# Optimization experiments

Hardware: AMD Instinct MI355X
Metric: run time of the kernel (lower is better)

The kernel has to match this reference:

```python
import jax, jax.numpy as jnp
import numpy as np

M, K, N = 131072, 1024, 512


def setup_inputs() -> dict:
    key = jax.random.key(0)
    k1, k2, k3, k4, k5 = jax.random.split(key, 5)
    scale = 0.02
    return {
        "x": jax.random.normal(k1, (M, K), dtype=jnp.float32),
        "w0": jax.random.uniform(k2, (K,), dtype=jnp.float32, minval=0.9, maxval=1.1),
        "w1": jax.random.normal(k3, (K, N), dtype=jnp.float32) * scale,
        "w2": jax.random.normal(k4, (K, N), dtype=jnp.float32) * scale,
        "w3": jax.random.normal(k5, (N, K), dtype=jnp.float32) * scale,
    }


def reference(x, w0, w1, w2, w3):
    # RMSNorm (no eps, matching the kernel): l = rsqrt(mean(x^2))
    l = jax.lax.rsqrt(jnp.sum(x * x, axis=-1) / K)          # [M]
    x1 = x * l[:, None] * w0[None, :]                        # [M, K]
    x2 = x1 @ w1                                             # gate   [M, N]
    y2 = x1 @ w2                                             # up     [M, N]
    x3 = jax.nn.silu(x2) * y2                                # SiLU-gate [M, N]
    out = x3 @ w3                                            # down   [M, K] (skip_connection=False)
    return out
```

## Files before the change

### kernel.cpp

```cpp
#include <hip/hip_runtime.h>
#include <cstdint>

typedef __attribute__((ext_vector_type(4))) float f32x4;
typedef __attribute__((ext_vector_type(8))) short bf16x8;
typedef __attribute__((ext_vector_type(4))) short bf16x4;

#define DEV static __device__ __forceinline__

DEV unsigned short f2bf(float f) {
    union { float f; unsigned int u; } v; v.f = f;
    unsigned int u = v.u;
    return (unsigned short)((u + 0x7FFFu + ((u >> 16) & 1u)) >> 16);
}

DEV void async_cp16(const void* g, void* l) {
    __builtin_amdgcn_global_load_lds(
        (const __attribute__((address_space(1))) unsigned int*)g,
        (__attribute__((address_space(3))) unsigned int*)l,
        16, 0, 0);
}

DEV void stage_half(const unsigned short* __restrict__ g, long kofs,
                    unsigned short* l, int tid, int gpitch) {
#pragma unroll
    for (int i = 0; i < 2; ++i) {
        int c = i * 512 + tid;
        int row = c >> 3;
        int ss = (c & 7) ^ (row & 7);
        async_cp16(g + (long)row * gpitch + kofs + ss * 8,
                   l + (i * 512 + (tid & 448)) * 8);
    }
}

template <int NT>
DEV void gemm256(const unsigned short* __restrict__ gA,
                 const unsigned short* __restrict__ gB,
                 const int gpitch, unsigned short* lds,
                 f32x4 (&acc)[8][4], const int tid) {
    const int lane = tid & 63;
    const int wv = tid >> 6;
    const int wr = wv >> 2;
    const int wcq = wv & 3;
    const int lhi = lane >> 4, llo = lane & 15;
    const int hb = wcq >> 1;
    const int br0 = (wcq & 1) * 64;

#define MFMA8(AF, BF, RI0, CJ0)                                               \
    _Pragma("unroll") for (int kq = 0; kq < 2; ++kq)                          \
    _Pragma("unroll") for (int i = 0; i < 4; ++i)                             \
    _Pragma("unroll") for (int j = 0; j < 2; ++j)                             \
        acc[RI0 + i][CJ0 + j] = __builtin_amdgcn_mfma_f32_16x16x32_bf16(      \
            AF[kq][i], BF[kq][j], acc[RI0 + i][CJ0 + j], 0, 0, 0);

#pragma unroll
    for (int h = 0; h < 2; ++h) {
        stage_half(gA + (long)h * 128 * gpitch, 0, lds + h * 8192, tid, gpitch);
        stage_half(gB + (long)h * 128 * gpitch, 0, lds + 32768 + h * 8192, tid, gpitch);
    }
    asm volatile("s_waitcnt vmcnt(0)" ::: "memory");
    __builtin_amdgcn_s_barrier();

    bf16x8 af[2][4], bf0[2][2], bf1[2][2];

    for (int kt = 0; kt < NT; ++kt) {
        const int cur = kt & 1, nxt = cur ^ 1;
        const unsigned short* lA = lds + (cur * 2 + wr) * 8192;
        const unsigned short* lB = lds + 32768 + (cur * 2 + hb) * 8192;
        const bool pf = (kt + 1 < NT);
        const long kofs = (long)(kt + 1) * 64;

#pragma unroll
        for (int kq = 0; kq < 2; ++kq) {
            const int q = kq * 4 + lhi;
#pragma unroll
            for (int i = 0; i < 4; ++i) {
                int r = i * 16 + llo;
                af[kq][i] = *(const bf16x8*)&lA[r * 64 + ((q ^ (r & 7)) << 3)];
            }
#pragma unroll
            for (int j = 0; j < 2; ++j) {
                int r = br0 + j * 16 + llo;
                bf0[kq][j] = *(const bf16x8*)&lB[r * 64 + ((q ^ (r & 7)) << 3)];
            }
        }
        if (pf) {
            stage_half(gA, kofs, lds + (nxt * 2 + 0) * 8192, tid, gpitch);
            stage_half(gA + (long)128 * gpitch, kofs, lds + (nxt * 2 + 1) * 8192, tid, gpitch);
        }
        __builtin_amdgcn_s_barrier();
        asm volatile("s_waitcnt lgkmcnt(0)");
        __builtin_amdgcn_sched_barrier(0);
        __builtin_amdgcn_s_setprio(1);
        MFMA8(af, bf0, 0, 0)
        __builtin_amdgcn_s_setprio(0);
        __builtin_amdgcn_s_barrier();

#pragma unroll
        for (int kq = 0; kq < 2; ++kq) {
            const int q = kq * 4 + lhi;
#pragma unroll
            for (int j = 0; j < 2; ++j) {
                int r = br0 + 32 + j * 16 + llo;
                bf1[kq][j] = *(const bf16x8*)&lB[r * 64 + ((q ^ (r & 7)) << 3)];
            }
        }
        if (pf) {
            stage_half(gB, kofs, lds + 32768 + (nxt * 2 + 0) * 8192, tid, gpitch);
            stage_half(gB + (long)128 * gpitch, kofs, lds + 32768 + (nxt * 2 + 1) * 8192, tid, gpitch);
        }
        __builtin_amdgcn_s_barrier();
        asm volatile("s_waitcnt lgkmcnt(0)");
        __builtin_amdgcn_sched_barrier(0);
        __builtin_amdgcn_s_setprio(1);
        MFMA8(af, bf1, 0, 2)
        __builtin_amdgcn_s_setprio(0);
        __builtin_amdgcn_s_barrier();

#pragma unroll
        for (int kq = 0; kq < 2; ++kq) {
            const int q = kq * 4 + lhi;
#pragma unroll
            for (int i = 0; i < 4; ++i) {
                int r = 64 + i * 16 + llo;
                af[kq][i] = *(const bf16x8*)&lA[r * 64 + ((q ^ (r & 7)) << 3)];
            }
        }
        __builtin_amdgcn_s_barrier();
        asm volatile("s_waitcnt lgkmcnt(0)");
        __builtin_amdgcn_sched_barrier(0);
        __builtin_amdgcn_s_setprio(1);
        MFMA8(af, bf0, 4, 0)
        __builtin_amdgcn_s_setprio(0);
        __builtin_amdgcn_s_barrier();

        __builtin_amdgcn_s_setprio(1);
        MFMA8(af, bf1, 4, 2)
        __builtin_amdgcn_s_setprio(0);
        if (pf) asm volatile("s_waitcnt vmcnt(0)" ::: "memory");
        __builtin_amdgcn_s_barrier();
        __builtin_amdgcn_sched_barrier(0);
    }
#undef MFMA8
}

__global__ void prep_w(const float* __restrict__ w0, const float* __restrict__ w1,
                       const float* __restrict__ w2, const float* __restrict__ w3,
                       unsigned short* __restrict__ w12t, unsigned short* __restrict__ w3t) {
    int t = blockIdx.x * 256 + threadIdx.x;
    if (t < 1048576) {
        int n = t >> 10, k = t & 1023;
        const float* src = (n & 1) ? w2 : w1;
        w12t[t] = f2bf(w0[k] * src[k * 512 + (n >> 1)]);
    } else {
        int idx = t - 1048576;
        int j = idx >> 9, n = idx & 511;
        w3t[idx] = f2bf(w3[n * 1024 + j]);
    }
}

__global__ __launch_bounds__(256)
void prep_x(const float* __restrict__ x, unsigned short* __restrict__ xb) {
    const int wv = threadIdx.x >> 6, lane = threadIdx.x & 63;
    const int stride = gridDim.x * 4;
    for (int row = blockIdx.x * 4 + wv; row < 131072; row += stride) {
        const float* xr = x + (long)row * 1024;
        f32x4 v[4];
        float s = 0.f;
#pragma unroll
        for (int c = 0; c < 4; ++c) {
            v[c] = *(const f32x4*)(xr + c * 256 + lane * 4);
            s += v[c].x * v[c].x + v[c].y * v[c].y + v[c].z * v[c].z + v[c].w * v[c].w;
        }
#pragma unroll
        for (int off = 32; off > 0; off >>= 1) s += __shfl_xor(s, off, 64);
        float l = rsqrtf(s * (1.0f / 1024.0f));
        unsigned short* xo = xb + (long)row * 1024;
#pragma unroll
        for (int c = 0; c < 4; ++c) {
            bf16x4 b;
            b.x = (short)f2bf(v[c].x * l);
            b.y = (short)f2bf(v[c].y * l);
            b.z = (short)f2bf(v[c].z * l);
            b.w = (short)f2bf(v[c].w * l);
            *(bf16x4*)(xo + c * 256 + lane * 4) = b;
        }
    }
}

__global__ __launch_bounds__(512, 2)
void gate_gemm(const unsigned short* __restrict__ xb,
               const unsigned short* __restrict__ w12t,
               unsigned short* __restrict__ x3) {
    __shared__ unsigned short lds[65536];
    const int tid = threadIdx.x;
    const int lane = tid & 63;
    const int wv = tid >> 6;
    const int wr = wv >> 2, wcq = wv & 3;
    const int lhi = lane >> 4, llo = lane & 15;

    int bid = blockIdx.x;
    int wgid = (bid & 7) * 256 + (bid >> 3);
    const int mt = wgid >> 2, nt = wgid & 3;

    f32x4 acc[8][4];
#pragma unroll
    for (int i = 0; i < 8; ++i)
#pragma unroll
        for (int j = 0; j < 4; ++j) acc[i][j] = (f32x4){0.f, 0.f, 0.f, 0.f};

    gemm256<16>(xb + (long)mt * 256 * 1024, w12t + (long)nt * 256 * 1024,
                1024, lds, acc, tid);

#pragma unroll
    for (int ri = 0; ri < 8; ++ri)
#pragma unroll
        for (int rr = 0; rr < 4; ++rr) {
            int R = wr * 128 + ri * 16 + lhi * 4 + rr;
#pragma unroll
            for (int cj = 0; cj < 4; ++cj) {
                float v = acc[ri][cj][rr];
                float p = __shfl_xor(v, 1, 64);
                float g = (lane & 1) ? p : v;
                float u = (lane & 1) ? v : p;
                float s = (g / (1.0f + __expf(-g))) * u;
                if (!(lane & 1))
                    lds[R * 136 + wcq * 32 + cj * 8 + (llo >> 1)] = f2bf(s);
            }
        }
    __syncthreads();
    unsigned short* xg = x3 + (long)(mt * 256) * 512 + nt * 128;
#pragma unroll
    for (int i = 0; i < 8; ++i) {
        int c = i * 512 + tid;
        int row = c >> 4, ch = c & 15;
        *(bf16x8*)(xg + (long)row * 512 + ch * 8) = *(const bf16x8*)&lds[row * 136 + ch * 8];
    }
}

__global__ __launch_bounds__(512, 2)
void down_gemm(const unsigned short* __restrict__ x3,
               const unsigned short* __restrict__ w3t,
               float* __restrict__ out) {
    __shared__ unsigned short lds[65536];
    const int tid = threadIdx.x;
    const int lane = tid & 63;
    const int wv = tid >> 6;
    const int wr = wv >> 2, wcq = wv & 3;
    const int lhi = lane >> 4, llo = lane & 15;

    int bid = blockIdx.x;
    int wgid = (bid & 7) * 256 + (bid >> 3);
    const int mt = wgid >> 2, nt = wgid & 3;

    f32x4 acc[8][4];
#pragma unroll
    for (int i = 0; i < 8; ++i)
#pragma unroll
        for (int j = 0; j < 4; ++j) acc[i][j] = (f32x4){0.f, 0.f, 0.f, 0.f};

    gemm256<8>(x3 + (long)mt * 256 * 512, w3t + (long)nt * 256 * 512,
               512, lds, acc, tid);

    float* op = out + (long)(mt * 256) * 1024 + nt * 256;
#pragma unroll
    for (int ri = 0; ri < 8; ++ri)
#pragma unroll
        for (int rr = 0; rr < 4; ++rr) {
            int R = wr * 128 + ri * 16 + lhi * 4 + rr;
#pragma unroll
            for (int cj = 0; cj < 4; ++cj)
                op[(long)R * 1024 + wcq * 64 + cj * 16 + llo] = acc[ri][cj][rr];
        }
}

extern "C" void kernel_launch(void* const* d_in, const int* in_sizes, int n_in,
                              void* d_out, int out_size, void* d_ws, size_t ws_size,
                              hipStream_t stream) {
    const float* x  = (const float*)d_in[0];
    const float* w0 = (const float*)d_in[1];
    const float* w1 = (const float*)d_in[2];
    const float* w2 = (const float*)d_in[3];
    const float* w3 = (const float*)d_in[4];
    float* out = (float*)d_out;

    unsigned short* w12t = (unsigned short*)d_ws;
    unsigned short* w3t  = w12t + 1024 * 1024;
    unsigned short* x3   = w3t + 1024 * 512;
    unsigned short* xb   = x3 + (size_t)131072 * 512;

    prep_w<<<dim3(6144), dim3(256), 0, stream>>>(w0, w1, w2, w3, w12t, w3t);
    prep_x<<<dim3(2048), dim3(256), 0, stream>>>(x, xb);
    gate_gemm<<<dim3(2048), dim3(512), 0, stream>>>(xb, w12t, x3);
    down_gemm<<<dim3(2048), dim3(512), 0, stream>>>(x3, w3t, out);
}
```

Measured before the change: 719.7 us.

## Stagger global-to-LDS prefetch across phases and deepen A prefetch by one tile

Spreads the four half-tile async loads for the next K step across the four MFMA phases instead of issuing them in two bursts. The first A half-tile is now fetched two iterations ahead into the current buffer once its reads are done, and partial vmcnt waits replace full drains. The aim is to overlap global memory latency with MFMA work and smooth issue pressure. It also changes the epilogue LDS row pitch from 136 to 144 to alter the bank mapping of the staging stores. The counted vmcnt waits depend on exactly how many load instructions stage_half issues, so a miscount could race.

```diff
diff --git a/kernel.cpp b/kernel.cpp
--- a/kernel.cpp
+++ b/kernel.cpp
@@ -52,12 +52,16 @@
         acc[RI0 + i][CJ0 + j] = __builtin_amdgcn_mfma_f32_16x16x32_bf16(      \
             AF[kq][i], BF[kq][j], acc[RI0 + i][CJ0 + j], 0, 0, 0);
 
-#pragma unroll
-    for (int h = 0; h < 2; ++h) {
-        stage_half(gA + (long)h * 128 * gpitch, 0, lds + h * 8192, tid, gpitch);
-        stage_half(gB + (long)h * 128 * gpitch, 0, lds + 32768 + h * 8192, tid, gpitch);
-    }
-    asm volatile("s_waitcnt vmcnt(0)" ::: "memory");
+    stage_half(gA, 0, lds + 0 * 8192, tid, gpitch);
+    stage_half(gA + (long)128 * gpitch, 0, lds + 1 * 8192, tid, gpitch);
+    stage_half(gB, 0, lds + 32768 + 0 * 8192, tid, gpitch);
+    stage_half(gB + (long)128 * gpitch, 0, lds + 32768 + 1 * 8192, tid, gpitch);
+    if (NT > 1) {
+        stage_half(gA, 64, lds + 2 * 8192, tid, gpitch);
+        asm volatile("s_waitcnt vmcnt(2)" ::: "memory");
+    } else {
+        asm volatile("s_waitcnt vmcnt(0)" ::: "memory");
+    }
     __builtin_amdgcn_s_barrier();
 
     bf16x8 af[2][4], bf0[2][2], bf1[2][2];
@@ -66,8 +70,10 @@
         const int cur = kt & 1, nxt = cur ^ 1;
         const unsigned short* lA = lds + (cur * 2 + wr) * 8192;
         const unsigned short* lB = lds + 32768 + (cur * 2 + hb) * 8192;
-        const bool pf = (kt + 1 < NT);
-        const long kofs = (long)(kt + 1) * 64;
+        const bool pf1 = (kt + 1 < NT);
+        const bool pf2 = (kt + 2 < NT);
+        const long k1 = (long)(kt + 1) * 64;
+        const long k2 = (long)(kt + 2) * 64;
 
 #pragma unroll
         for (int kq = 0; kq < 2; ++kq) {
@@ -83,10 +89,8 @@
                 bf0[kq][j] = *(const bf16x8*)&lB[r * 64 + ((q ^ (r & 7)) << 3)];
             }
         }
-        if (pf) {
-            stage_half(gA, kofs, lds + (nxt * 2 + 0) * 8192, tid, gpitch);
-            stage_half(gA + (long)128 * gpitch, kofs, lds + (nxt * 2 + 1) * 8192, tid, gpitch);
-        }
+        if (pf1)
+            stage_half(gA + (long)128 * gpitch, k1, lds + (nxt * 2 + 1) * 8192, tid, gpitch);
         __builtin_amdgcn_s_barrier();
         asm volatile("s_waitcnt lgkmcnt(0)");
         __builtin_amdgcn_sched_barrier(0);
@@ -104,10 +108,8 @@
                 bf1[kq][j] = *(const bf16x8*)&lB[r * 64 + ((q ^ (r & 7)) << 3)];
             }
         }
-        if (pf) {
-            stage_half(gB, kofs, lds + 32768 + (nxt * 2 + 0) * 8192, tid, gpitch);
-            stage_half(gB + (long)128 * gpitch, kofs, lds + 32768 + (nxt * 2 + 1) * 8192, tid, gpitch);
-        }
+        if (pf1)
+            stage_half(gB, k1, lds + 32768 + (nxt * 2 + 0) * 8192, tid, gpitch);
         __builtin_amdgcn_s_barrier();
         asm volatile("s_waitcnt lgkmcnt(0)");
         __builtin_amdgcn_sched_barrier(0);
@@ -125,6 +127,8 @@
                 af[kq][i] = *(const bf16x8*)&lA[r * 64 + ((q ^ (r & 7)) << 3)];
             }
         }
+        if (pf1)
+            stage_half(gB + (long)128 * gpitch, k1, lds + 32768 + (nxt * 2 + 1) * 8192, tid, gpitch);
         __builtin_amdgcn_s_barrier();
         asm volatile("s_waitcnt lgkmcnt(0)");
         __builtin_amdgcn_sched_barrier(0);
@@ -133,10 +137,15 @@
         __builtin_amdgcn_s_setprio(0);
         __builtin_amdgcn_s_barrier();
 
+        if (pf2)
+            stage_half(gA, k2, lds + (cur * 2 + 0) * 8192, tid, gpitch);
         __builtin_amdgcn_s_setprio(1);
         MFMA8(af, bf1, 4, 2)
         __builtin_amdgcn_s_setprio(0);
-        if (pf) asm volatile("s_waitcnt vmcnt(0)" ::: "memory");
+        if (pf1) {
+            if (pf2) asm volatile("s_waitcnt vmcnt(2)" ::: "memory");
+            else     asm volatile("s_waitcnt vmcnt(0)" ::: "memory");
+        }
         __builtin_amdgcn_s_barrier();
         __builtin_amdgcn_sched_barrier(0);
     }
@@ -224,7 +233,7 @@
                 float u = (lane & 1) ? v : p;
                 float s = (g / (1.0f + __expf(-g))) * u;
                 if (!(lane & 1))
-                    lds[R * 136 + wcq * 32 + cj * 8 + (llo >> 1)] = f2bf(s);
+                    lds[R * 144 + wcq * 32 + cj * 8 + (llo >> 1)] = f2bf(s);
             }
         }
     __syncthreads();
@@ -233,7 +242,7 @@
     for (int i = 0; i < 8; ++i) {
         int c = i * 512 + tid;
         int row = c >> 4, ch = c & 15;
-        *(bf16x8*)(xg + (long)row * 512 + ch * 8) = *(const bf16x8*)&lds[row * 136 + ch * 8];
+        *(bf16x8*)(xg + (long)row * 512 + ch * 8) = *(const bf16x8*)&lds[row * 144 + ch * 8];
     }
 }
 
```

After: 703.0 us. 1.02x faster.
